# Kernel optimization log

Measured on AMD Instinct MI355X. Metric: run time of the kernel, lower is better.

Reference implementation:

```python
import jax, jax.numpy as jnp
import numpy as np

NEG_SLOPE = 0.01  # torch F.leaky_relu default


def _graph_conv(x, W, b, src, dst, n_dst):
    """DGL GraphConv, norm='both': out = D_dst^{-1/2} A^T (D_src^{-1/2} x W) + b.
    Degrees clamped to min 1 (DGL behavior). src/dst are edge endpoint indices.
    """
    n_src = x.shape[0]
    ones = jnp.ones(src.shape[0], dtype=x.dtype)
    out_deg = jnp.zeros(n_src, dtype=x.dtype).at[src].add(ones)
    in_deg = jnp.zeros(n_dst, dtype=x.dtype).at[dst].add(ones)
    inv_s = jax.lax.rsqrt(jnp.maximum(out_deg, 1.0))
    inv_d = jax.lax.rsqrt(jnp.maximum(in_deg, 1.0))
    # weight first (in_feats >= out_feats path in DGL; math identical either way)
    feat = (x * inv_s[:, None]) @ W                      # [n_src, out]
    agg = jax.ops.segment_sum(feat[src], dst, num_segments=n_dst)  # SpMM
    return agg * inv_d[:, None] + b


def setup_inputs() -> dict:
    key = jax.random.key(0)
    ks = jax.random.split(key, 16)
    Nc, Ng, F, H, O = 50000, 30000, 128, 128, 128
    Ecc, Ecg, Egc = 500000, 400000, 400000
    inp = {
        "x_chem": jax.random.normal(ks[0], (Nc, F), jnp.float32),
        "x_gene": jax.random.normal(ks[1], (Ng, F), jnp.float32),
        "src_cc": jax.random.randint(ks[2], (Ecc,), 0, Nc, jnp.int32),
        "dst_cc": jax.random.randint(ks[3], (Ecc,), 0, Nc, jnp.int32),
        "src_cg": jax.random.randint(ks[4], (Ecg,), 0, Nc, jnp.int32),
        "dst_cg": jax.random.randint(ks[5], (Ecg,), 0, Ng, jnp.int32),
        "src_gc": jax.random.randint(ks[6], (Egc,), 0, Ng, jnp.int32),
        "dst_gc": jax.random.randint(ks[7], (Egc,), 0, Nc, jnp.int32),
    }
    scale1 = 1.0 / np.sqrt(F)
    scale2 = 1.0 / np.sqrt(H)
    inp["W1_cc"] = jax.random.normal(ks[8], (F, H), jnp.float32) * scale1
    inp["W1_cg"] = jax.random.normal(ks[9], (F, H), jnp.float32) * scale1
    inp["W1_gc"] = jax.random.normal(ks[10], (F, H), jnp.float32) * scale1
    inp["W2_cc"] = jax.random.normal(ks[11], (H, O), jnp.float32) * scale2
    inp["W2_cg"] = jax.random.normal(ks[12], (H, O), jnp.float32) * scale2
    inp["W2_gc"] = jax.random.normal(ks[13], (H, O), jnp.float32) * scale2
    for name, d in [("b1_cc", H), ("b1_cg", H), ("b1_gc", H), ("b2_cc", O), ("b2_cg", O), ("b2_gc", O)]:
        inp[name] = jnp.zeros((d,), jnp.float32)
    return inp


def reference(x_chem, x_gene, src_cc, dst_cc, src_cg, dst_cg, src_gc, dst_gc,
              W1_cc, b1_cc, W1_cg, b1_cg, W1_gc, b1_gc,
              W2_cc, b2_cc, W2_cg, b2_cg, W2_gc, b2_gc):
    Nc, Ng = x_chem.shape[0], x_gene.shape[0]
    # --- layer 1: HeteroGraphConv with sum aggregation across relations ---
    h1_chem = (_graph_conv(x_chem, W1_cc, b1_cc, src_cc, dst_cc, Nc)
               + _graph_conv(x_gene, W1_gc, b1_gc, src_gc, dst_gc, Nc))
    h1_gene = _graph_conv(x_chem, W1_cg, b1_cg, src_cg, dst_cg, Ng)
    h1_chem = jax.nn.leaky_relu(h1_chem, NEG_SLOPE)
    h1_gene = jax.nn.leaky_relu(h1_gene, NEG_SLOPE)
    # --- layer 2 ---
    h2_chem = (_graph_conv(h1_chem, W2_cc, b2_cc, src_cc, dst_cc, Nc)
               + _graph_conv(h1_gene, W2_gc, b2_gc, src_gc, dst_gc, Nc))
    return h2_chem
```

## Files before the change

kernel.cpp:

```cpp
#include <hip/hip_runtime.h>
#include <math.h>

#define NEG_SLOPE 0.01f
#define ELLW 40

typedef float f4 __attribute__((ext_vector_type(4)));
typedef __bf16 bf16x8 __attribute__((ext_vector_type(8)));
typedef __bf16 bf16x4 __attribute__((ext_vector_type(4)));

__global__ __launch_bounds__(256) void prep_w(
    const float* __restrict__ W0, const float* __restrict__ W1,
    const float* __restrict__ W2, const float* __restrict__ W3,
    const float* __restrict__ W4, __bf16* __restrict__ H, __bf16* __restrict__ L)
{
    const int y = blockIdx.y;
    const float* W = y == 0 ? W0 : y == 1 ? W1 : y == 2 ? W2 : y == 3 ? W3 : W4;
    int idx = blockIdx.x * 256 + threadIdx.x;
    int k = idx >> 7, n = idx & 127;
    float w = W[idx];
    __bf16 h = (__bf16)w;
    __bf16 l = (__bf16)(w - (float)h);
    H[(size_t)y * 16384 + n * 128 + k] = h;
    L[(size_t)y * 16384 + n * 128 + k] = l;
}

template <int RELU>
__device__ __forceinline__ void gemm_core(const float* __restrict__ A,
    const __bf16* __restrict__ Bh, const __bf16* __restrict__ Bl,
    float* __restrict__ C, int M, int row0, int tid,
    __bf16 (*Ah)[136], __bf16 (*Al)[136])
{
#pragma unroll
    for (int it = 0; it < 8; ++it) {
        int idx4 = it * 256 + tid;
        int r = idx4 >> 5;
        int c = (idx4 & 31) << 2;
        int rg = row0 + r;
        f4 v = {0.f, 0.f, 0.f, 0.f};
        if (rg < M) v = *(const f4*)(A + (size_t)rg * 128 + c);
        if (RELU) {
#pragma unroll
            for (int j = 0; j < 4; ++j) v[j] = v[j] >= 0.f ? v[j] : v[j] * NEG_SLOPE;
        }
        bf16x4 hv, lv;
#pragma unroll
        for (int j = 0; j < 4; ++j) {
            __bf16 h = (__bf16)v[j];
            hv[j] = h;
            lv[j] = (__bf16)(v[j] - (float)h);
        }
        *(bf16x4*)&Ah[r][c] = hv;
        *(bf16x4*)&Al[r][c] = lv;
    }
    __syncthreads();

    const int lane = tid & 63;
    const int wid = tid >> 6;
    const int lm = lane & 15;
    const int lq = lane >> 4;
    const int mbase = (wid & 1) * 32;
    const int nbase = (wid >> 1) * 64;

    f4 acc[2][4] = {};
#pragma unroll
    for (int kc = 0; kc < 4; ++kc) {
        const int koff = kc * 32 + lq * 8;
        bf16x8 ah[2], al[2], bh[4], bl[4];
#pragma unroll
        for (int mi = 0; mi < 2; ++mi) {
            ah[mi] = *(const bf16x8*)&Ah[mbase + mi * 16 + lm][koff];
            al[mi] = *(const bf16x8*)&Al[mbase + mi * 16 + lm][koff];
        }
#pragma unroll
        for (int ni = 0; ni < 4; ++ni) {
            size_t boff = (size_t)(nbase + ni * 16 + lm) * 128 + koff;
            bh[ni] = *(const bf16x8*)(Bh + boff);
            bl[ni] = *(const bf16x8*)(Bl + boff);
        }
#pragma unroll
        for (int mi = 0; mi < 2; ++mi)
#pragma unroll
            for (int ni = 0; ni < 4; ++ni) {
                acc[mi][ni] = __builtin_amdgcn_mfma_f32_16x16x32_bf16(ah[mi], bh[ni], acc[mi][ni], 0, 0, 0);
                acc[mi][ni] = __builtin_amdgcn_mfma_f32_16x16x32_bf16(al[mi], bh[ni], acc[mi][ni], 0, 0, 0);
                acc[mi][ni] = __builtin_amdgcn_mfma_f32_16x16x32_bf16(ah[mi], bl[ni], acc[mi][ni], 0, 0, 0);
            }
    }

#pragma unroll
    for (int mi = 0; mi < 2; ++mi) {
        int rbase = row0 + mbase + mi * 16 + lq * 4;
#pragma unroll
        for (int r = 0; r < 4; ++r) {
            int row = rbase + r;
            if (row < M) {
#pragma unroll
                for (int ni = 0; ni < 4; ++ni)
                    C[(size_t)row * 128 + nbase + ni * 16 + lm] = acc[mi][ni][r];
            }
        }
    }
}

__global__ __launch_bounds__(256) void fused_build_gemm(
    const int* __restrict__ s0, const int* __restrict__ d0, int* sd0, int* c0, int* e0, int E0, int B0,
    const int* __restrict__ s1, const int* __restrict__ d1, int* sd1, int* c1, int* e1, int E1, int B1,
    const int* __restrict__ s2, const int* __restrict__ d2, int* sd2, int* c2, int* e2, int E2,
    const float* __restrict__ xc, const float* __restrict__ xg,
    const __bf16* __restrict__ wt_h, const __bf16* __restrict__ wt_l,
    float* __restrict__ t_cg, float* __restrict__ t_cc, float* __restrict__ t_gc,
    int Nc, int Ng, int gBc, int G, int EB)
{
    __shared__ __bf16 Ah[64][136];
    __shared__ __bf16 Al[64][136];
    const int idx = blockIdx.x;
    const int r7 = idx % 7, q = idx / 7;
    if (r7 < 2) {
        int g = q * 2 + r7;
        if (g >= G) return;
        if (g < gBc)
            gemm_core<0>(xc, wt_h, wt_l, t_cg, Nc, g * 64, threadIdx.x, Ah, Al);
        else if (g < 2 * gBc)
            gemm_core<0>(xc, wt_h + 16384, wt_l + 16384, t_cc, Nc, (g - gBc) * 64, threadIdx.x, Ah, Al);
        else
            gemm_core<0>(xg, wt_h + 2 * 16384, wt_l + 2 * 16384, t_gc, Ng, (g - 2 * gBc) * 64, threadIdx.x, Ah, Al);
    } else {
        int eb = q * 5 + (r7 - 2);
        if (eb >= EB) return;
        const int* src; const int* dst; int* sdeg; int* cnt; int* ell; int E; int base;
        if (eb < B0)            { src = s0; dst = d0; sdeg = sd0; cnt = c0; ell = e0; E = E0; base = eb; }
        else if (eb < B0 + B1)  { src = s1; dst = d1; sdeg = sd1; cnt = c1; ell = e1; E = E1; base = eb - B0; }
        else                    { src = s2; dst = d2; sdeg = sd2; cnt = c2; ell = e2; E = E2; base = eb - B0 - B1; }
        int i = base * 256 + threadIdx.x;
        if (i < E) {
            int s = src[i];
            int d = dst[i];
            atomicAdd(&sdeg[s], 1);
            int p = atomicAdd(&cnt[d], 1);
            if (p < ELLW) ell[d * ELLW + p] = s;
        }
    }
}

__global__ __launch_bounds__(256) void gemm2_both(
    const float* __restrict__ h1c, const float* __restrict__ h1g,
    const __bf16* __restrict__ wt_h, const __bf16* __restrict__ wt_l,
    float* __restrict__ t_cc, float* __restrict__ t_gc, int Nc, int Ng, int gBc)
{
    __shared__ __bf16 Ah[64][136];
    __shared__ __bf16 Al[64][136];
    if ((int)blockIdx.x < gBc)
        gemm_core<1>(h1c, wt_h + 3 * 16384, wt_l + 3 * 16384, t_cc, Nc, blockIdx.x * 64, threadIdx.x, Ah, Al);
    else
        gemm_core<1>(h1g, wt_h + 4 * 16384, wt_l + 4 * 16384, t_gc, Ng, (blockIdx.x - gBc) * 64, threadIdx.x, Ah, Al);
}

__device__ __forceinline__ void rel_accum(const float* __restrict__ feat,
    const int* __restrict__ cp, int n, const int* __restrict__ sdeg, int c2,
    float& a0, float& a1)
{
    int i = 0;
    for (; i + 3 < n; i += 4) {
        int q0 = cp[i], q1 = cp[i + 1], q2 = cp[i + 2], q3 = cp[i + 3];
        float w0 = rsqrtf(fmaxf((float)sdeg[q0], 1.0f));
        float w1 = rsqrtf(fmaxf((float)sdeg[q1], 1.0f));
        float w2 = rsqrtf(fmaxf((float)sdeg[q2], 1.0f));
        float w3 = rsqrtf(fmaxf((float)sdeg[q3], 1.0f));
        float2 v0 = *(const float2*)(feat + (size_t)q0 * 128 + c2);
        float2 v1 = *(const float2*)(feat + (size_t)q1 * 128 + c2);
        float2 v2 = *(const float2*)(feat + (size_t)q2 * 128 + c2);
        float2 v3 = *(const float2*)(feat + (size_t)q3 * 128 + c2);
        a0 = fmaf(v0.x, w0, a0); a1 = fmaf(v0.y, w0, a1);
        a0 = fmaf(v1.x, w1, a0); a1 = fmaf(v1.y, w1, a1);
        a0 = fmaf(v2.x, w2, a0); a1 = fmaf(v2.y, w2, a1);
        a0 = fmaf(v3.x, w3, a0); a1 = fmaf(v3.y, w3, a1);
    }
    for (; i < n; ++i) {
        int q0 = cp[i];
        float w0 = rsqrtf(fmaxf((float)sdeg[q0], 1.0f));
        float2 v0 = *(const float2*)(feat + (size_t)q0 * 128 + c2);
        a0 = fmaf(v0.x, w0, a0); a1 = fmaf(v0.y, w0, a1);
    }
}

__global__ __launch_bounds__(256) void gather_l1(
    const float* __restrict__ t_cg, const int* __restrict__ ell_cg,
    const int* __restrict__ cnt_cg, const int* __restrict__ degs_cg,
    const float* __restrict__ f_cc, const int* __restrict__ ell_cc,
    const int* __restrict__ cnt_cc, const int* __restrict__ degs_cc,
    const float* __restrict__ t_gc, const int* __restrict__ ell_gc,
    const int* __restrict__ cnt_gc, const int* __restrict__ degs_gc,
    const float* __restrict__ b1_cg, const float* __restrict__ b1_cc, const float* __restrict__ b1_gc,
    float* __restrict__ h1_gene, float* __restrict__ h1_chem, int Ng, int Nc, int Bg)
{
    int lane = threadIdx.x & 63;
    int c2 = lane * 2;
    if ((int)blockIdx.x < Bg) {
        int row = blockIdx.x * 4 + (threadIdx.x >> 6);
        if (row >= Ng) return;
        int n = cnt_cg[row];
        float wd = rsqrtf(fmaxf((float)n, 1.0f));
        if (n > ELLW) n = ELLW;
        float a0 = 0.f, a1 = 0.f;
        rel_accum(t_cg, ell_cg + row * ELLW, n, degs_cg, c2, a0, a1);
        float r0 = fmaf(a0, wd, b1_cg[c2]);
        float r1 = fmaf(a1, wd, b1_cg[c2 + 1]);
        *(float2*)(h1_gene + (size_t)row * 128 + c2) = make_float2(r0, r1);
    } else {
        int row = (blockIdx.x - Bg) * 4 + (threadIdx.x >> 6);
        if (row >= Nc) return;
        int na = cnt_cc[row];
        float wa = rsqrtf(fmaxf((float)na, 1.0f));
        if (na > ELLW) na = ELLW;
        float a0 = 0.f, a1 = 0.f;
        rel_accum(f_cc, ell_cc + row * ELLW, na, degs_cc, c2, a0, a1);
        float r0 = fmaf(a0, wa, b1_cc[c2]);
        float r1 = fmaf(a1, wa, b1_cc[c2 + 1]);
        int nb = cnt_gc[row];
        float wb = rsqrtf(fmaxf((float)nb, 1.0f));
        if (nb > ELLW) nb = ELLW;
        float s0 = 0.f, s1 = 0.f;
        rel_accum(t_gc, ell_gc + row * ELLW, nb, degs_gc, c2, s0, s1);
        r0 += fmaf(s0, wb, b1_gc[c2]);
        r1 += fmaf(s1, wb, b1_gc[c2 + 1]);
        *(float2*)(h1_chem + (size_t)row * 128 + c2) = make_float2(r0, r1);
    }
}

__global__ __launch_bounds__(256) void gather_l2(
    const float* __restrict__ fA, const int* __restrict__ ellA,
    const int* __restrict__ cntA, const int* __restrict__ degsA,
    const float* __restrict__ fB, const int* __restrict__ ellB,
    const int* __restrict__ cntB, const int* __restrict__ degsB,
    const float* __restrict__ bA, const float* __restrict__ bB,
    float* __restrict__ out, int Nd)
{
    int lane = threadIdx.x & 63;
    int c2 = lane * 2;
    int row = blockIdx.x * 4 + (threadIdx.x >> 6);
    if (row >= Nd) return;
    int na = cntA[row];
    float wa = rsqrtf(fmaxf((float)na, 1.0f));
    if (na > ELLW) na = ELLW;
    float a0 = 0.f, a1 = 0.f;
    rel_accum(fA, ellA + row * ELLW, na, degsA, c2, a0, a1);
    float r0 = fmaf(a0, wa, bA[c2]);
    float r1 = fmaf(a1, wa, bA[c2 + 1]);
    int nb = cntB[row];
    float wb = rsqrtf(fmaxf((float)nb, 1.0f));
    if (nb > ELLW) nb = ELLW;
    float s0 = 0.f, s1 = 0.f;
    rel_accum(fB, ellB + row * ELLW, nb, degsB, c2, s0, s1);
    r0 += fmaf(s0, wb, bB[c2]);
    r1 += fmaf(s1, wb, bB[c2 + 1]);
    *(float2*)(out + (size_t)row * 128 + c2) = make_float2(r0, r1);
}

extern "C" void kernel_launch(void* const* d_in, const int* in_sizes, int n_in,
                              void* d_out, int out_size, void* d_ws, size_t ws_size,
                              hipStream_t stream)
{
    const float* x_chem = (const float*)d_in[0];
    const float* x_gene = (const float*)d_in[1];
    const int* src_cc = (const int*)d_in[2];
    const int* dst_cc = (const int*)d_in[3];
    const int* src_cg = (const int*)d_in[4];
    const int* dst_cg = (const int*)d_in[5];
    const int* src_gc = (const int*)d_in[6];
    const int* dst_gc = (const int*)d_in[7];
    const float* W1_cc = (const float*)d_in[8];
    const float* W1_cg = (const float*)d_in[9];
    const float* W1_gc = (const float*)d_in[10];
    const float* W2_cc = (const float*)d_in[11];
    const float* W2_gc = (const float*)d_in[13];
    const float* b1_cc = (const float*)d_in[14];
    const float* b1_cg = (const float*)d_in[15];
    const float* b1_gc = (const float*)d_in[16];
    const float* b2_cc = (const float*)d_in[17];
    const float* b2_gc = (const float*)d_in[19];
    (void)n_in; (void)out_size; (void)ws_size;

    const int Nc = in_sizes[0] / 128;
    const int Ng = in_sizes[1] / 128;
    const int Ecc = in_sizes[2];
    const int Ecg = in_sizes[4];
    const int Egc = in_sizes[6];

    int* ip = (int*)d_ws;
    int* cnt_cc  = ip; ip += Nc;
    int* cnt_cg  = ip; ip += Ng;
    int* cnt_gc  = ip; ip += Nc;
    int* degs_cc = ip; ip += Nc;
    int* degs_cg = ip; ip += Nc;
    int* degs_gc = ip; ip += Ng;
    const int degTotal = 4 * Nc + 2 * Ng;
    int* ell_cc = ip; ip += (size_t)Nc * ELLW;
    int* ell_cg = ip; ip += (size_t)Ng * ELLW;
    int* ell_gc = ip; ip += (size_t)Nc * ELLW;
    size_t intCount = (size_t)(ip - (int*)d_ws);
    intCount = (intCount + 3) & ~(size_t)3;
    float* fp = (float*)d_ws + intCount;
    float* h1_chem = fp; fp += (size_t)Nc * 128;
    float* h1_gene = fp; fp += (size_t)Ng * 128;
    float* tmp_cg  = fp; fp += (size_t)Nc * 128;
    float* tmp_gc  = fp; fp += (size_t)Ng * 128;
    __bf16* wt_h = (__bf16*)fp;
    __bf16* wt_l = wt_h + 5 * 16384;
    float* outF = (float*)d_out;

    hipMemsetAsync(d_ws, 0, (size_t)degTotal * sizeof(int), stream);

    dim3 blk(256);
    const int B0 = (Ecc + 255) / 256, B1 = (Ecg + 255) / 256, B2 = (Egc + 255) / 256;
    const int EB = B0 + B1 + B2;
    const int gBc = (Nc + 63) / 64, gBg = (Ng + 63) / 64;
    const int G = 2 * gBc + gBg;
    int Q = (G + 1) / 2;
    if ((EB + 4) / 5 > Q) Q = (EB + 4) / 5;
    const int T = 7 * Q;

    prep_w<<<dim3(64, 5), blk, 0, stream>>>(W1_cg, W1_cc, W1_gc, W2_cc, W2_gc, wt_h, wt_l);

    fused_build_gemm<<<T, blk, 0, stream>>>(
        src_cc, dst_cc, degs_cc, cnt_cc, ell_cc, Ecc, B0,
        src_cg, dst_cg, degs_cg, cnt_cg, ell_cg, Ecg, B1,
        src_gc, dst_gc, degs_gc, cnt_gc, ell_gc, Egc,
        x_chem, x_gene, wt_h, wt_l, tmp_cg, outF, tmp_gc,
        Nc, Ng, gBc, G, EB);

    const int Bg = (Ng + 3) / 4, Bc = (Nc + 3) / 4;
    gather_l1<<<Bg + Bc, blk, 0, stream>>>(
        tmp_cg, ell_cg, cnt_cg, degs_cg,
        outF,  ell_cc, cnt_cc, degs_cc,
        tmp_gc, ell_gc, cnt_gc, degs_gc,
        b1_cg, b1_cc, b1_gc, h1_gene, h1_chem, Ng, Nc, Bg);

    gemm2_both<<<gBc + gBg, blk, 0, stream>>>(h1_chem, h1_gene, wt_h, wt_l,
        tmp_cg, tmp_gc, Nc, Ng, gBc);

    gather_l2<<<Bc, blk, 0, stream>>>(
        tmp_cg, ell_cc, cnt_cc, degs_cc,
        tmp_gc, ell_gc, cnt_gc, degs_gc,
        b2_cc, b2_gc, outF, Nc);
}
```

Before: 443.5 us.

## Gather with float4 lanes split across edge halves; fold memset into prep kernel

The gather kernels now have each wavefront split into two halves. Each half loads 16-byte float4 feature slices for alternating edges, and the two partial sums are combined with a cross-half shuffle before a single half writes the row. Separately, the degree-counter memset is merged into the weight-prep kernel as extra blocks, which removes one launch. The wider loads aim to cut per-edge instruction count and raise memory-level parallelism in the bandwidth-bound SpMM gather, at the cost of the shuffle reduction and half the lanes sitting idle during the store.

```diff
diff --git a/kernel.cpp b/kernel.cpp
--- a/kernel.cpp
+++ b/kernel.cpp
@@ -8,20 +8,27 @@
 typedef __bf16 bf16x8 __attribute__((ext_vector_type(8)));
 typedef __bf16 bf16x4 __attribute__((ext_vector_type(4)));
 
-__global__ __launch_bounds__(256) void prep_w(
+__global__ __launch_bounds__(256) void prep_w_zero(
     const float* __restrict__ W0, const float* __restrict__ W1,
     const float* __restrict__ W2, const float* __restrict__ W3,
-    const float* __restrict__ W4, __bf16* __restrict__ H, __bf16* __restrict__ L)
-{
-    const int y = blockIdx.y;
-    const float* W = y == 0 ? W0 : y == 1 ? W1 : y == 2 ? W2 : y == 3 ? W3 : W4;
-    int idx = blockIdx.x * 256 + threadIdx.x;
-    int k = idx >> 7, n = idx & 127;
-    float w = W[idx];
-    __bf16 h = (__bf16)w;
-    __bf16 l = (__bf16)(w - (float)h);
-    H[(size_t)y * 16384 + n * 128 + k] = h;
-    L[(size_t)y * 16384 + n * 128 + k] = l;
+    const float* __restrict__ W4, __bf16* __restrict__ H, __bf16* __restrict__ L,
+    int* __restrict__ zp, int zN)
+{
+    const int b = blockIdx.x;
+    if (b < 320) {
+        const int y = b >> 6;
+        const float* W = y == 0 ? W0 : y == 1 ? W1 : y == 2 ? W2 : y == 3 ? W3 : W4;
+        int idx = (b & 63) * 256 + threadIdx.x;
+        int k = idx >> 7, n = idx & 127;
+        float w = W[idx];
+        __bf16 h = (__bf16)w;
+        __bf16 l = (__bf16)(w - (float)h);
+        H[(size_t)y * 16384 + n * 128 + k] = h;
+        L[(size_t)y * 16384 + n * 128 + k] = l;
+    } else {
+        int i = (b - 320) * 256 + threadIdx.x;
+        if (i < zN) zp[i] = 0;
+    }
 }
 
 template <int RELU>
@@ -155,32 +162,36 @@
         gemm_core<1>(h1g, wt_h + 4 * 16384, wt_l + 4 * 16384, t_gc, Ng, (blockIdx.x - gBc) * 64, threadIdx.x, Ah, Al);
 }
 
-__device__ __forceinline__ void rel_accum(const float* __restrict__ feat,
-    const int* __restrict__ cp, int n, const int* __restrict__ sdeg, int c2,
-    float& a0, float& a1)
-{
-    int i = 0;
-    for (; i + 3 < n; i += 4) {
-        int q0 = cp[i], q1 = cp[i + 1], q2 = cp[i + 2], q3 = cp[i + 3];
+__device__ __forceinline__ void rel_accum4(const float* __restrict__ feat,
+    const int* __restrict__ cp, int n, const int* __restrict__ sdeg,
+    int half, int c4, f4& acc)
+{
+    int i = half;
+    for (; i + 2 < n; i += 4) {
+        int q0 = cp[i], q1 = cp[i + 2];
         float w0 = rsqrtf(fmaxf((float)sdeg[q0], 1.0f));
         float w1 = rsqrtf(fmaxf((float)sdeg[q1], 1.0f));
-        float w2 = rsqrtf(fmaxf((float)sdeg[q2], 1.0f));
-        float w3 = rsqrtf(fmaxf((float)sdeg[q3], 1.0f));
-        float2 v0 = *(const float2*)(feat + (size_t)q0 * 128 + c2);
-        float2 v1 = *(const float2*)(feat + (size_t)q1 * 128 + c2);
-        float2 v2 = *(const float2*)(feat + (size_t)q2 * 128 + c2);
-        float2 v3 = *(const float2*)(feat + (size_t)q3 * 128 + c2);
-        a0 = fmaf(v0.x, w0, a0); a1 = fmaf(v0.y, w0, a1);
-        a0 = fmaf(v1.x, w1, a0); a1 = fmaf(v1.y, w1, a1);
-        a0 = fmaf(v2.x, w2, a0); a1 = fmaf(v2.y, w2, a1);
-        a0 = fmaf(v3.x, w3, a0); a1 = fmaf(v3.y, w3, a1);
-    }
-    for (; i < n; ++i) {
+        f4 v0 = *(const f4*)(feat + (size_t)q0 * 128 + c4);
+        f4 v1 = *(const f4*)(feat + (size_t)q1 * 128 + c4);
+        acc += v0 * w0;
+        acc += v1 * w1;
+    }
+    if (i < n) {
         int q0 = cp[i];
         float w0 = rsqrtf(fmaxf((float)sdeg[q0], 1.0f));
-        float2 v0 = *(const float2*)(feat + (size_t)q0 * 128 + c2);
-        a0 = fmaf(v0.x, w0, a0); a1 = fmaf(v0.y, w0, a1);
-    }
+        f4 v0 = *(const f4*)(feat + (size_t)q0 * 128 + c4);
+        acc += v0 * w0;
+    }
+}
+
+__device__ __forceinline__ f4 xhalf_sum(f4 r)
+{
+    f4 o;
+    o[0] = __shfl_xor(r[0], 32);
+    o[1] = __shfl_xor(r[1], 32);
+    o[2] = __shfl_xor(r[2], 32);
+    o[3] = __shfl_xor(r[3], 32);
+    return r + o;
 }
 
 __global__ __launch_bounds__(256) void gather_l1(
@@ -193,37 +204,43 @@
     const float* __restrict__ b1_cg, const float* __restrict__ b1_cc, const float* __restrict__ b1_gc,
     float* __restrict__ h1_gene, float* __restrict__ h1_chem, int Ng, int Nc, int Bg)
 {
-    int lane = threadIdx.x & 63;
-    int c2 = lane * 2;
+    const int lane = threadIdx.x & 63;
+    const int half = lane >> 5;
+    const int c4 = (lane & 31) << 2;
     if ((int)blockIdx.x < Bg) {
         int row = blockIdx.x * 4 + (threadIdx.x >> 6);
         if (row >= Ng) return;
         int n = cnt_cg[row];
         float wd = rsqrtf(fmaxf((float)n, 1.0f));
         if (n > ELLW) n = ELLW;
-        float a0 = 0.f, a1 = 0.f;
-        rel_accum(t_cg, ell_cg + row * ELLW, n, degs_cg, c2, a0, a1);
-        float r0 = fmaf(a0, wd, b1_cg[c2]);
-        float r1 = fmaf(a1, wd, b1_cg[c2 + 1]);
-        *(float2*)(h1_gene + (size_t)row * 128 + c2) = make_float2(r0, r1);
+        f4 acc = {0.f, 0.f, 0.f, 0.f};
+        rel_accum4(t_cg, ell_cg + row * ELLW, n, degs_cg, half, c4, acc);
+        f4 r = acc * wd;
+        r = xhalf_sum(r);
+        if (half == 0) {
+            r += *(const f4*)(b1_cg + c4);
+            *(f4*)(h1_gene + (size_t)row * 128 + c4) = r;
+        }
     } else {
         int row = (blockIdx.x - Bg) * 4 + (threadIdx.x >> 6);
         if (row >= Nc) return;
         int na = cnt_cc[row];
         float wa = rsqrtf(fmaxf((float)na, 1.0f));
         if (na > ELLW) na = ELLW;
-        float a0 = 0.f, a1 = 0.f;
-        rel_accum(f_cc, ell_cc + row * ELLW, na, degs_cc, c2, a0, a1);
-        float r0 = fmaf(a0, wa, b1_cc[c2]);
-        float r1 = fmaf(a1, wa, b1_cc[c2 + 1]);
+        f4 accA = {0.f, 0.f, 0.f, 0.f};
+        rel_accum4(f_cc, ell_cc + row * ELLW, na, degs_cc, half, c4, accA);
         int nb = cnt_gc[row];
         float wb = rsqrtf(fmaxf((float)nb, 1.0f));
         if (nb > ELLW) nb = ELLW;
-        float s0 = 0.f, s1 = 0.f;
-        rel_accum(t_gc, ell_gc + row * ELLW, nb, degs_gc, c2, s0, s1);
-        r0 += fmaf(s0, wb, b1_gc[c2]);
-        r1 += fmaf(s1, wb, b1_gc[c2 + 1]);
-        *(float2*)(h1_chem + (size_t)row * 128 + c2) = make_float2(r0, r1);
+        f4 accB = {0.f, 0.f, 0.f, 0.f};
+        rel_accum4(t_gc, ell_gc + row * ELLW, nb, degs_gc, half, c4, accB);
+        f4 r = accA * wa + accB * wb;
+        r = xhalf_sum(r);
+        if (half == 0) {
+            r += *(const f4*)(b1_cc + c4);
+            r += *(const f4*)(b1_gc + c4);
+            *(f4*)(h1_chem + (size_t)row * 128 + c4) = r;
+        }
     }
 }
 
@@ -235,25 +252,28 @@
     const float* __restrict__ bA, const float* __restrict__ bB,
     float* __restrict__ out, int Nd)
 {
-    int lane = threadIdx.x & 63;
-    int c2 = lane * 2;
+    const int lane = threadIdx.x & 63;
+    const int half = lane >> 5;
+    const int c4 = (lane & 31) << 2;
     int row = blockIdx.x * 4 + (threadIdx.x >> 6);
     if (row >= Nd) return;
     int na = cntA[row];
     float wa = rsqrtf(fmaxf((float)na, 1.0f));
     if (na > ELLW) na = ELLW;
-    float a0 = 0.f, a1 = 0.f;
-    rel_accum(fA, ellA + row * ELLW, na, degsA, c2, a0, a1);
-    float r0 = fmaf(a0, wa, bA[c2]);
-    float r1 = fmaf(a1, wa, bA[c2 + 1]);
+    f4 accA = {0.f, 0.f, 0.f, 0.f};
+    rel_accum4(fA, ellA + row * ELLW, na, degsA, half, c4, accA);
     int nb = cntB[row];
     float wb = rsqrtf(fmaxf((float)nb, 1.0f));
     if (nb > ELLW) nb = ELLW;
-    float s0 = 0.f, s1 = 0.f;
-    rel_accum(fB, ellB + row * ELLW, nb, degsB, c2, s0, s1);
-    r0 += fmaf(s0, wb, bB[c2]);
-    r1 += fmaf(s1, wb, bB[c2 + 1]);
-    *(float2*)(out + (size_t)row * 128 + c2) = make_float2(r0, r1);
+    f4 accB = {0.f, 0.f, 0.f, 0.f};
+    rel_accum4(fB, ellB + row * ELLW, nb, degsB, half, c4, accB);
+    f4 r = accA * wa + accB * wb;
+    r = xhalf_sum(r);
+    if (half == 0) {
+        r += *(const f4*)(bA + c4);
+        r += *(const f4*)(bB + c4);
+        *(f4*)(out + (size_t)row * 128 + c4) = r;
+    }
 }
 
 extern "C" void kernel_launch(void* const* d_in, const int* in_sizes, int n_in,
@@ -308,8 +328,6 @@
     __bf16* wt_l = wt_h + 5 * 16384;
     float* outF = (float*)d_out;
 
-    hipMemsetAsync(d_ws, 0, (size_t)degTotal * sizeof(int), stream);
-
     dim3 blk(256);
     const int B0 = (Ecc + 255) / 256, B1 = (Ecg + 255) / 256, B2 = (Egc + 255) / 256;
     const int EB = B0 + B1 + B2;
@@ -319,7 +337,9 @@
     if ((EB + 4) / 5 > Q) Q = (EB + 4) / 5;
     const int T = 7 * Q;
 
-    prep_w<<<dim3(64, 5), blk, 0, stream>>>(W1_cg, W1_cc, W1_gc, W2_cc, W2_gc, wt_h, wt_l);
+    const int zB = (degTotal + 255) / 256;
+    prep_w_zero<<<320 + zB, blk, 0, stream>>>(W1_cg, W1_cc, W1_gc, W2_cc, W2_gc,
+        wt_h, wt_l, (int*)d_ws, degTotal);
 
     fused_build_gemm<<<T, blk, 0, stream>>>(
         src_cc, dst_cc, degs_cc, cnt_cc, ell_cc, Ecc, B0,
```

Result: no change. 435.1 us (-1.9%).
